# Optimization experiments

Measured on AMD Instinct MI355X. Metric: run time of the kernel, lower is better.

## Reference

```python
import jax, jax.numpy as jnp
import numpy as np

B, N, D, H = 2, 2048, 768, 12
HD = D // H  # head_dim = 64
SCALE = HD ** -0.5


def setup_inputs() -> dict:
    key = jax.random.key(0)
    ks = jax.random.split(key, 8)
    return {
        "x": jax.random.normal(ks[0], (B, N, D), jnp.float32),
        "masks": jax.random.uniform(ks[1], (B, H, N), jnp.float32),
        "lambda_r": jax.random.uniform(ks[2], (B, H), jnp.float32) * 4.0 + 1.0,
        "theta_r": jax.random.uniform(ks[3], (B, H), jnp.float32),
        "mask_weights": jax.random.uniform(ks[4], (B, H), jnp.float32),
        "qkv_w": jax.random.normal(ks[5], (D, 3 * D), jnp.float32) * (D ** -0.5),
        "qkv_b": jnp.zeros((3 * D,), jnp.float32),
        "proj_w": jax.random.normal(ks[6], (D, D), jnp.float32) * (D ** -0.5),
        "proj_b": jnp.zeros((D,), jnp.float32),
    }


def reference(x, masks, lambda_r, theta_r, mask_weights, qkv_w, qkv_b, proj_w, proj_b):
    # qkv projection: [B,N,3D] -> [3,B,H,N,HD]
    qkv = (x @ qkv_w + qkv_b).reshape(B, N, 3, H, HD).transpose(2, 0, 3, 1, 4)
    q, k, v = qkv[0], qkv[1], qkv[2]
    # raw scores [B,H,N,N]
    attn = jnp.einsum('bhqd,bhkd->bhqk', q, k) * SCALE
    # region gate: sigmoid(lambda * (m_i*m_j - theta)) multiplied into scores pre-softmax
    gate = jax.nn.sigmoid(
        lambda_r[:, :, None, None]
        * (masks[:, :, :, None] * masks[:, :, None, :] - theta_r[:, :, None, None])
    )
    attn = jax.nn.softmax(attn * gate, axis=-1)  # dropout is identity in eval
    out = jnp.einsum('bhqk,bhkd->bqhd', attn, v).reshape(B, N, D)
    # per-head output scaling via mask_weights
    out = out * jnp.repeat(mask_weights, HD, axis=-1)[:, None, :]
    return out @ proj_w + proj_b
```

## Files before the change

### kernel.cpp

```cpp
#include <hip/hip_runtime.h>

typedef unsigned short u16;
typedef unsigned int u32;
typedef __attribute__((ext_vector_type(8))) short short8;
typedef __attribute__((ext_vector_type(4))) float f32x4;

#define NB 2
#define NSEQ 2048
#define DIM 768
#define NH 12
#define HDIM 64

#define LOG2E 1.44269504088896f
#define CFOLD 0.18033688f

#if defined(__has_builtin)
#if __has_builtin(__builtin_amdgcn_exp2f)
#define EXPB(x) __builtin_amdgcn_exp2f(x)
#else
#define EXPB(x) exp2f(x)
#endif
#if __has_builtin(__builtin_amdgcn_rcpf)
#define RCP(x) __builtin_amdgcn_rcpf(x)
#else
#define RCP(x) (1.0f / (x))
#endif
#else
#define EXPB(x) exp2f(x)
#define RCP(x) (1.0f / (x))
#endif

__device__ __forceinline__ u16 f2bf(float x) {
    union { float f; unsigned u; } v; v.f = x;
    unsigned r = v.u + 0x7fffu + ((v.u >> 16) & 1u);
    return (u16)(r >> 16);
}

__device__ __forceinline__ u32 pack_bf16(float a, float b) {
    union { float f; u32 u; } A, B; A.f = a; B.f = b;
    u32 ra = A.u + 0x7fffu + ((A.u >> 16) & 1u);
    u32 rb = B.u + 0x7fffu + ((B.u >> 16) & 1u);
    return __builtin_amdgcn_perm(rb, ra, 0x07060302u);
}

__device__ __forceinline__ u32 pack_rtn(float a, float b) {
    union { float f; u32 u; } A, B; A.f = a; B.f = b;
    return __builtin_amdgcn_perm(B.u + 0x8000u, A.u + 0x8000u, 0x07060302u);
}

__device__ __forceinline__ f32x4 mfma16(short8 a, short8 b, f32x4 c) {
    return __builtin_amdgcn_mfma_f32_16x16x32_bf16(a, b, c, 0, 0, 0);
}

__device__ __forceinline__ void glds16(const u16* g, u16* l) {
    __builtin_amdgcn_global_load_lds((const __attribute__((address_space(1))) u32*)g,
                                     (__attribute__((address_space(3))) u32*)l, 16, 0, 0);
}

__global__ __launch_bounds__(256) void prep(const float* __restrict__ x, u16* __restrict__ xb,
                                            const float* __restrict__ qkv_w, u16* __restrict__ wq,
                                            const float* __restrict__ proj_w, u16* __restrict__ wp) {
    const int t = threadIdx.x;
    int bid = blockIdx.x;
    if (bid < 3072) {
        int i = (bid * 256 + t) * 4;
        float4 v = *(const float4*)(x + i);
        *(uint2*)(xb + i) = make_uint2(pack_bf16(v.x, v.y), pack_bf16(v.z, v.w));
        return;
    }
    const float* in; u16* outp; int rows, cols, bx, by;
    if (bid < 3072 + 1728) {
        bid -= 3072; in = qkv_w; outp = wq; rows = 768; cols = 2304;
        bx = bid % 72; by = bid / 72;
    } else {
        bid -= 4800; in = proj_w; outp = wp; rows = 768; cols = 768;
        bx = bid % 24; by = bid / 24;
    }
    __shared__ float tile[32][33];
    int c0 = bx * 32, r0 = by * 32;
    int tx = t & 31, ty = t >> 5;
    #pragma unroll
    for (int i = 0; i < 32; i += 8)
        tile[ty + i][tx] = in[(size_t)(r0 + ty + i) * cols + c0 + tx];
    __syncthreads();
    #pragma unroll
    for (int i = 0; i < 32; i += 8)
        outp[(size_t)(c0 + ty + i) * rows + r0 + tx] = f2bf(tile[tx][ty + i]);
}

__global__ __launch_bounds__(256) void gemm_qkv(const u16* __restrict__ A,
                                                const u16* __restrict__ BT,
                                                const float* __restrict__ bias,
                                                u16* __restrict__ qo,
                                                u16* __restrict__ ko,
                                                u16* __restrict__ vo) {
    __shared__ __align__(16) u16 pool[17408];
    const int bm = blockIdx.y * 128, bn = blockIdx.x * 128;
    const int t = threadIdx.x;
    const int lane = t & 63, wave = t >> 6;
    const int l15 = lane & 15, quad = lane >> 4;
    const int wm = (wave >> 1) * 64, wn = (wave & 1) * 64;

    const int srow = t >> 2;
    const int sc = (t & 3) ^ ((srow >> 1) & 3);
    const u16* ga = A + (size_t)(bm + srow) * DIM + sc * 8;
    const u16* gb = BT + (size_t)(bn + srow) * DIM + sc * 8;
    const int ldst = wave * 512;
    const int swz = (quad ^ ((l15 >> 1) & 3)) * 8;
    u16* As0 = pool;
    u16* Bs0 = pool + 8192;

    f32x4 acc[4][4] = {};
    glds16(ga, As0 + ldst); glds16(ga + (size_t)64 * DIM, As0 + 2048 + ldst);
    glds16(gb, Bs0 + ldst); glds16(gb + (size_t)64 * DIM, Bs0 + 2048 + ldst);
    ga += 32; gb += 32;

    const int NKT = DIM / 32;
    for (int kt = 0; kt < NKT; kt++) {
        const int bo = (kt & 1) * 4096;
        __syncthreads();
        if (kt + 1 < NKT) {
            const int bn2 = (bo ^ 4096);
            glds16(ga, As0 + bn2 + ldst); glds16(ga + (size_t)64 * DIM, As0 + bn2 + 2048 + ldst);
            glds16(gb, Bs0 + bn2 + ldst); glds16(gb + (size_t)64 * DIM, Bs0 + bn2 + 2048 + ldst);
            ga += 32; gb += 32;
        }
        short8 af[4], bf[4];
        #pragma unroll
        for (int i = 0; i < 4; i++) af[i] = *(const short8*)&As0[bo + (wm + i * 16 + l15) * 32 + swz];
        #pragma unroll
        for (int j = 0; j < 4; j++) bf[j] = *(const short8*)&Bs0[bo + (wn + j * 16 + l15) * 32 + swz];
        #pragma unroll
        for (int i = 0; i < 4; i++)
            #pragma unroll
            for (int j = 0; j < 4; j++)
                acc[i][j] = mfma16(af[i], bf[j], acc[i][j]);
    }

    __syncthreads();
    u16* Cs = pool;
    #pragma unroll
    for (int i = 0; i < 4; i++) {
        int row0 = wm + i * 16 + quad * 4;
        #pragma unroll
        for (int j = 0; j < 4; j++) {
            int lcol = wn + j * 16 + l15;
            float bb = bias[bn + lcol];
            #pragma unroll
            for (int r = 0; r < 4; r++)
                Cs[(row0 + r) * 136 + lcol] = f2bf(acc[i][j][r] + bb);
        }
    }
    __syncthreads();

    const int w = bn / DIM;
    const int h0 = (bn - w * DIM) >> 6;
    const int b = bm >> 11, nnb = bm & 2047;
    if (w < 2) {
        u16* dst = w ? ko : qo;
        #pragma unroll
        for (int p = 0; p < 8; p++) {
            int row = p * 16 + (t >> 4);
            int chunk = t & 15;
            short8 v = *(const short8*)&Cs[row * 136 + chunk * 8];
            *(short8*)&dst[(((size_t)(b * NH + h0 + (chunk >> 3))) * NSEQ + nnb + row) * HDIM +
                           (chunk & 7) * 8] = v;
        }
    } else {
        #pragma unroll
        for (int p = 0; p < 8; p++) {
            int hdf = p * 16 + (t >> 4);
            int nn0 = (t & 15) * 8;
            short8 v;
            #pragma unroll
            for (int k = 0; k < 8; k++) v[k] = (short)Cs[(nn0 + k) * 136 + hdf];
            *(short8*)&vo[(((size_t)(b * NH + h0 + (hdf >> 6))) * HDIM + (hdf & 63)) * NSEQ +
                          nnb + nn0] = v;
        }
    }
}

__global__ __launch_bounds__(256) void attn_kernel(const u16* __restrict__ Q,
                                                   const u16* __restrict__ Kg,
                                                   const u16* __restrict__ Vt,
                                                   const float* __restrict__ masks,
                                                   const float* __restrict__ lambda_r,
                                                   const float* __restrict__ theta_r,
                                                   const float* __restrict__ mask_w,
                                                   u16* __restrict__ AO) {
    const int bh = blockIdx.y;
    const int b = bh / NH, h = bh % NH;
    const int qb = blockIdx.x * 64;
    const int t = threadIdx.x, wave = t >> 6, lane = t & 63;
    const int l15 = lane & 15, quad = lane >> 4;

    __shared__ __align__(16) u16 Ks[2][4096];
    __shared__ __align__(16) u16 Vs[2][4096];
    __shared__ __align__(16) u16 Ps[4][1152];
    __shared__ __align__(16) float mks[2][64];

    const float lam = lambda_r[bh], th = theta_r[bh], mw = mask_w[bh];
    const float Bfac = lam * th * LOG2E;

    const size_t base = (size_t)bh * (NSEQ * HDIM);
    const int qrow = qb + wave * 16;

    const u16* Qr = Q + base + (size_t)(qrow + l15) * HDIM;
    short8 bq0 = *(const short8*)(Qr + quad * 8);
    short8 bq1 = *(const short8*)(Qr + 32 + quad * 8);
    const float Afac = -lam * LOG2E * masks[bh * NSEQ + qrow + l15];

    const int srow = t >> 3;
    const int gc = (t & 7) ^ (srow & 7);
    const u16* kgp = Kg + base + (size_t)srow * HDIM + gc * 8;
    const u16* vgp = Vt + base + (size_t)srow * NSEQ + gc * 8;
    const int ldst = wave * 512;

    const int ph = (quad ^ (l15 & 7)) * 8;
    const int kb0 = l15 * 64 + ph, kb1 = l15 * 64 + (ph ^ 32);
    u16* PsW = Ps[wave];
    const int pw = l15 * 72 + quad * 4;
    const int prd = l15 * 72 + quad * 8;
    const float* mrow = masks + bh * NSEQ;

    float lsum = 0.f;
    f32x4 O[4] = {};

    glds16(kgp, &Ks[0][ldst]);
    glds16(kgp + 32 * HDIM, &Ks[0][2048 + ldst]);
    glds16(vgp, &Vs[0][ldst]);
    glds16(vgp + (size_t)32 * NSEQ, &Vs[0][2048 + ldst]);
    if (t < 16) *(float4*)&mks[0][t * 4] = *(const float4*)&mrow[t * 4];

    const int NT = NSEQ / 64;
    for (int kt = 0; kt < NT; kt++) {
        const int buf = kt & 1;
        __syncthreads();
        if (kt + 1 < NT) {
            const u16* kn = kgp + (kt + 1) * 64 * HDIM;
            const u16* vn = vgp + (kt + 1) * 64;
            glds16(kn, &Ks[buf ^ 1][ldst]);
            glds16(kn + 32 * HDIM, &Ks[buf ^ 1][2048 + ldst]);
            glds16(vn, &Vs[buf ^ 1][ldst]);
            glds16(vn + (size_t)32 * NSEQ, &Vs[buf ^ 1][2048 + ldst]);
            if (t < 16) *(float4*)&mks[buf ^ 1][t * 4] = *(const float4*)&mrow[(kt + 1) * 64 + t * 4];
        }
        const u16* KsB = Ks[buf];
        const u16* VsB = Vs[buf];
        const float* mkb = mks[buf];

        float gp[4][4];
        #pragma unroll
        for (int c = 0; c < 4; c++) {
            float4 mkv = *(const float4*)&mkb[c * 16 + quad * 4];
            #pragma unroll
            for (int r = 0; r < 4; r++) {
                float mk = (r == 0) ? mkv.x : (r == 1) ? mkv.y : (r == 2) ? mkv.z : mkv.w;
                float e = EXPB(fmaf(mk, Afac, Bfac));
                gp[c][r] = CFOLD * RCP(1.0f + e);
            }
        }

        #pragma unroll
        for (int c = 0; c < 4; c++) {
            short8 ak0 = *(const short8*)&KsB[kb0 + c * 1024];
            short8 ak1 = *(const short8*)&KsB[kb1 + c * 1024];
            f32x4 S = {0.f, 0.f, 0.f, 0.f};
            S = mfma16(ak0, bq0, S);
            S = mfma16(ak1, bq1, S);
            float p[4];
            #pragma unroll
            for (int r = 0; r < 4; r++) p[r] = EXPB(S[r] * gp[c][r]);
            lsum += (p[0] + p[1]) + (p[2] + p[3]);
            *(uint2*)&PsW[pw + c * 16] = make_uint2(pack_rtn(p[0], p[1]), pack_rtn(p[2], p[3]));
        }

        #pragma unroll
        for (int kc = 0; kc < 2; kc++) {
            const int vb = kc ? kb1 : kb0;
            short8 bp = *(const short8*)&PsW[prd + kc * 32];
            #pragma unroll
            for (int dt = 0; dt < 4; dt++) {
                short8 av = *(const short8*)&VsB[vb + dt * 1024];
                O[dt] = mfma16(av, bp, O[dt]);
            }
        }
    }

    lsum += __shfl_xor(lsum, 16);
    lsum += __shfl_xor(lsum, 32);
    float sc = mw / lsum;
    u16* aor = AO + ((size_t)(b * NSEQ) + qrow + l15) * DIM + h * HDIM + quad * 4;
    #pragma unroll
    for (int dt = 0; dt < 4; dt++) {
        *(uint2*)(aor + dt * 16) = make_uint2(pack_rtn(O[dt][0] * sc, O[dt][1] * sc),
                                              pack_rtn(O[dt][2] * sc, O[dt][3] * sc));
    }
}

__global__ __launch_bounds__(256) void gemm_proj(const u16* __restrict__ A,
                                                 const u16* __restrict__ BT,
                                                 const float* __restrict__ bias,
                                                 float* __restrict__ outp) {
    __shared__ __align__(16) u16 As[2][4096];
    __shared__ __align__(16) u16 Bs[2][2048];
    const int bm = blockIdx.y * 128, bn = blockIdx.x * 64;
    const int t = threadIdx.x;
    const int lane = t & 63, wave = t >> 6;
    const int l15 = lane & 15, quad = lane >> 4;
    const int wm = wave * 32;

    const int srow = t >> 2;
    const int sc = (t & 3) ^ ((srow >> 1) & 3);
    const u16* ga = A + (size_t)(bm + srow) * DIM + sc * 8;
    const u16* gb = BT + (size_t)(bn + srow) * DIM + sc * 8;
    const int ldst = wave * 512;
    const int swz = (quad ^ ((l15 >> 1) & 3)) * 8;

    f32x4 acc[2][4] = {};
    glds16(ga, &As[0][ldst]); glds16(ga + (size_t)64 * DIM, &As[0][2048 + ldst]);
    glds16(gb, &Bs[0][ldst]);
    ga += 32; gb += 32;

    const int NKT = DIM / 32;
    for (int kt = 0; kt < NKT; kt++) {
        const int buf = kt & 1;
        __syncthreads();
        if (kt + 1 < NKT) {
            glds16(ga, &As[buf ^ 1][ldst]); glds16(ga + (size_t)64 * DIM, &As[buf ^ 1][2048 + ldst]);
            glds16(gb, &Bs[buf ^ 1][ldst]);
            ga += 32; gb += 32;
        }
        short8 af[2], bf[4];
        #pragma unroll
        for (int i = 0; i < 2; i++) af[i] = *(const short8*)&As[buf][(wm + i * 16 + l15) * 32 + swz];
        #pragma unroll
        for (int j = 0; j < 4; j++) bf[j] = *(const short8*)&Bs[buf][(j * 16 + l15) * 32 + swz];
        #pragma unroll
        for (int i = 0; i < 2; i++)
            #pragma unroll
            for (int j = 0; j < 4; j++)
                acc[i][j] = mfma16(af[i], bf[j], acc[i][j]);
    }

    #pragma unroll
    for (int i = 0; i < 2; i++) {
        int mr = bm + wm + i * 16 + quad * 4;
        #pragma unroll
        for (int j = 0; j < 4; j++) {
            int ncol = bn + j * 16 + l15;
            float bb = bias[ncol];
            #pragma unroll
            for (int r = 0; r < 4; r++)
                outp[(size_t)(mr + r) * DIM + ncol] = acc[i][j][r] + bb;
        }
    }
}

extern "C" void kernel_launch(void* const* d_in, const int* in_sizes, int n_in,
                              void* d_out, int out_size, void* d_ws, size_t ws_size,
                              hipStream_t stream) {
    const float* x            = (const float*)d_in[0];
    const float* masks        = (const float*)d_in[1];
    const float* lambda_r     = (const float*)d_in[2];
    const float* theta_r      = (const float*)d_in[3];
    const float* mask_weights = (const float*)d_in[4];
    const float* qkv_w        = (const float*)d_in[5];
    const float* qkv_b        = (const float*)d_in[6];
    const float* proj_w       = (const float*)d_in[7];
    const float* proj_b       = (const float*)d_in[8];
    float* outp = (float*)d_out;

    const size_t SZH = (size_t)NB * NH * NSEQ * HDIM;
    u16* xb    = (u16*)d_ws;
    u16* wqkvT = xb + (size_t)4096 * 768;
    u16* wprT  = wqkvT + (size_t)2304 * 768;
    u16* qg    = wprT + (size_t)768 * 768;
    u16* kg    = qg + SZH;
    u16* vt    = kg + SZH;
    u16* ao    = xb;

    prep<<<dim3(3072 + 1728 + 576), 256, 0, stream>>>(x, xb, qkv_w, wqkvT, proj_w, wprT);
    gemm_qkv<<<dim3(2304 / 128, 4096 / 128), 256, 0, stream>>>(xb, wqkvT, qkv_b, qg, kg, vt);
    attn_kernel<<<dim3(NSEQ / 64, NB * NH), 256, 0, stream>>>(qg, kg, vt, masks, lambda_r,
                                                              theta_r, mask_weights, ao);
    gemm_proj<<<dim3(768 / 64, 4096 / 128), 256, 0, stream>>>(ao, wprT, proj_b, outp);
}
```

Measured before the change: 192.4 us.

## Split attention key tiles across wave pairs with LDS reduction of partial outputs

The attention kernel goes to 512 threads. Each pair of waves shares one 16-row query group, and each wave of the pair handles half of every 64-key tile. The partial O accumulators and row sums are combined through shared memory at the end, with one wave of each pair doing the normalised store. This doubles the waves per block and halves each wave's per-tile work to expose more parallelism and latency hiding, at the cost of an extra LDS reduction, more syncs and higher register/LDS pressure per block.

Measured after the change: 186.6 us. 1.03x faster.

```diff
diff --git a/kernel.cpp b/kernel.cpp
--- a/kernel.cpp
+++ b/kernel.cpp
@@ -180,7 +180,7 @@
     }
 }
 
-__global__ __launch_bounds__(256) void attn_kernel(const u16* __restrict__ Q,
+__global__ __launch_bounds__(512) void attn_kernel(const u16* __restrict__ Q,
                                                    const u16* __restrict__ Kg,
                                                    const u16* __restrict__ Vt,
                                                    const float* __restrict__ masks,
@@ -193,17 +193,18 @@
     const int qb = blockIdx.x * 64;
     const int t = threadIdx.x, wave = t >> 6, lane = t & 63;
     const int l15 = lane & 15, quad = lane >> 4;
-
-    __shared__ __align__(16) u16 Ks[2][4096];
-    __shared__ __align__(16) u16 Vs[2][4096];
-    __shared__ __align__(16) u16 Ps[4][1152];
+    const int g = wave >> 1, kh = wave & 1;
+
+    __shared__ __align__(16) u16 pool[16384];
+    __shared__ __align__(16) u16 Ps[8][640];
     __shared__ __align__(16) float mks[2][64];
+    __shared__ float Ls[8][16];
 
     const float lam = lambda_r[bh], th = theta_r[bh], mw = mask_w[bh];
     const float Bfac = lam * th * LOG2E;
 
     const size_t base = (size_t)bh * (NSEQ * HDIM);
-    const int qrow = qb + wave * 16;
+    const int qrow = qb + g * 16;
 
     const u16* Qr = Q + base + (size_t)(qrow + l15) * HDIM;
     short8 bq0 = *(const short8*)(Qr + quad * 8);
@@ -214,45 +215,40 @@
     const int gc = (t & 7) ^ (srow & 7);
     const u16* kgp = Kg + base + (size_t)srow * HDIM + gc * 8;
     const u16* vgp = Vt + base + (size_t)srow * NSEQ + gc * 8;
-    const int ldst = wave * 512;
+    const int wbase = wave * 512;
 
     const int ph = (quad ^ (l15 & 7)) * 8;
-    const int kb0 = l15 * 64 + ph, kb1 = l15 * 64 + (ph ^ 32);
+    const int vph = kh ? (ph ^ 32) : ph;
     u16* PsW = Ps[wave];
-    const int pw = l15 * 72 + quad * 4;
-    const int prd = l15 * 72 + quad * 8;
+    const int pw = l15 * 40 + quad * 4;
+    const int prd = l15 * 40 + quad * 8;
     const float* mrow = masks + bh * NSEQ;
 
     float lsum = 0.f;
     f32x4 O[4] = {};
 
-    glds16(kgp, &Ks[0][ldst]);
-    glds16(kgp + 32 * HDIM, &Ks[0][2048 + ldst]);
-    glds16(vgp, &Vs[0][ldst]);
-    glds16(vgp + (size_t)32 * NSEQ, &Vs[0][2048 + ldst]);
+    glds16(kgp, pool + wbase);
+    glds16(vgp, pool + 8192 + wbase);
     if (t < 16) *(float4*)&mks[0][t * 4] = *(const float4*)&mrow[t * 4];
 
     const int NT = NSEQ / 64;
     for (int kt = 0; kt < NT; kt++) {
-        const int buf = kt & 1;
+        const int bufofs = (kt & 1) * 4096;
         __syncthreads();
         if (kt + 1 < NT) {
-            const u16* kn = kgp + (kt + 1) * 64 * HDIM;
-            const u16* vn = vgp + (kt + 1) * 64;
-            glds16(kn, &Ks[buf ^ 1][ldst]);
-            glds16(kn + 32 * HDIM, &Ks[buf ^ 1][2048 + ldst]);
-            glds16(vn, &Vs[buf ^ 1][ldst]);
-            glds16(vn + (size_t)32 * NSEQ, &Vs[buf ^ 1][2048 + ldst]);
-            if (t < 16) *(float4*)&mks[buf ^ 1][t * 4] = *(const float4*)&mrow[(kt + 1) * 64 + t * 4];
-        }
-        const u16* KsB = Ks[buf];
-        const u16* VsB = Vs[buf];
-        const float* mkb = mks[buf];
-
-        float gp[4][4];
-        #pragma unroll
-        for (int c = 0; c < 4; c++) {
-            float4 mkv = *(const float4*)&mkb[c * 16 + quad * 4];
+            glds16(kgp + (kt + 1) * 64 * HDIM, pool + (bufofs ^ 4096) + wbase);
+            glds16(vgp + (kt + 1) * 64, pool + 8192 + (bufofs ^ 4096) + wbase);
+            if (t < 16) *(float4*)&mks[(kt + 1) & 1][t * 4] =
+                *(const float4*)&mrow[(kt + 1) * 64 + t * 4];
+        }
+        const u16* KsB = pool + bufofs;
+        const u16* VsB = pool + 8192 + bufofs;
+        const float* mkb = mks[kt & 1];
+
+        float gp[2][4];
+        #pragma unroll
+        for (int c = 0; c < 2; c++) {
+            float4 mkv = *(const float4*)&mkb[kh * 32 + c * 16 + quad * 4];
             #pragma unroll
             for (int r = 0; r < 4; r++) {
                 float mk = (r == 0) ? mkv.x : (r == 1) ? mkv.y : (r == 2) ? mkv.z : mkv.w;
@@ -262,9 +258,10 @@
         }
 
         #pragma unroll
-        for (int c = 0; c < 4; c++) {
-            short8 ak0 = *(const short8*)&KsB[kb0 + c * 1024];
-            short8 ak1 = *(const short8*)&KsB[kb1 + c * 1024];
+        for (int c = 0; c < 2; c++) {
+            const int krow = kh * 32 + c * 16 + l15;
+            short8 ak0 = *(const short8*)&KsB[krow * 64 + ph];
+            short8 ak1 = *(const short8*)&KsB[krow * 64 + (ph ^ 32)];
             f32x4 S = {0.f, 0.f, 0.f, 0.f};
             S = mfma16(ak0, bq0, S);
             S = mfma16(ak1, bq1, S);
@@ -275,26 +272,35 @@
             *(uint2*)&PsW[pw + c * 16] = make_uint2(pack_rtn(p[0], p[1]), pack_rtn(p[2], p[3]));
         }
 
-        #pragma unroll
-        for (int kc = 0; kc < 2; kc++) {
-            const int vb = kc ? kb1 : kb0;
-            short8 bp = *(const short8*)&PsW[prd + kc * 32];
-            #pragma unroll
-            for (int dt = 0; dt < 4; dt++) {
-                short8 av = *(const short8*)&VsB[vb + dt * 1024];
-                O[dt] = mfma16(av, bp, O[dt]);
-            }
-        }
-    }
-
-    lsum += __shfl_xor(lsum, 16);
-    lsum += __shfl_xor(lsum, 32);
-    float sc = mw / lsum;
-    u16* aor = AO + ((size_t)(b * NSEQ) + qrow + l15) * DIM + h * HDIM + quad * 4;
-    #pragma unroll
-    for (int dt = 0; dt < 4; dt++) {
-        *(uint2*)(aor + dt * 16) = make_uint2(pack_rtn(O[dt][0] * sc, O[dt][1] * sc),
-                                              pack_rtn(O[dt][2] * sc, O[dt][3] * sc));
+        short8 bp = *(const short8*)&PsW[prd];
+        #pragma unroll
+        for (int dt = 0; dt < 4; dt++) {
+            short8 av = *(const short8*)&VsB[(dt * 16 + l15) * 64 + vph];
+            O[dt] = mfma16(av, bp, O[dt]);
+        }
+    }
+
+    __syncthreads();
+    float* Op = (float*)pool;
+    const int slot = (wave * 64 + lane) * 16;
+    #pragma unroll
+    for (int dt = 0; dt < 4; dt++) *(f32x4*)&Op[slot + dt * 4] = O[dt];
+    float ls = lsum;
+    ls += __shfl_xor(ls, 16);
+    ls += __shfl_xor(ls, 32);
+    if (quad == 0) Ls[wave][l15] = ls;
+    __syncthreads();
+    if (kh == 0) {
+        const int pslot = ((wave ^ 1) * 64 + lane) * 16;
+        float sc = mw / (ls + Ls[wave ^ 1][l15]);
+        u16* aor = AO + ((size_t)(b * NSEQ) + qrow + l15) * DIM + h * HDIM + quad * 4;
+        #pragma unroll
+        for (int dt = 0; dt < 4; dt++) {
+            f32x4 oc = *(const f32x4*)&Op[pslot + dt * 4];
+            float o0 = (O[dt][0] + oc[0]) * sc, o1 = (O[dt][1] + oc[1]) * sc;
+            float o2 = (O[dt][2] + oc[2]) * sc, o3 = (O[dt][3] + oc[3]) * sc;
+            *(uint2*)(aor + dt * 16) = make_uint2(pack_rtn(o0, o1), pack_rtn(o2, o3));
+        }
     }
 }
 
@@ -382,7 +388,7 @@
 
     prep<<<dim3(3072 + 1728 + 576), 256, 0, stream>>>(x, xb, qkv_w, wqkvT, proj_w, wprT);
     gemm_qkv<<<dim3(2304 / 128, 4096 / 128), 256, 0, stream>>>(xb, wqkvT, qkv_b, qg, kg, vt);
-    attn_kernel<<<dim3(NSEQ / 64, NB * NH), 256, 0, stream>>>(qg, kg, vt, masks, lambda_r,
+    attn_kernel<<<dim3(NSEQ / 64, NB * NH), 512, 0, stream>>>(qg, kg, vt, masks, lambda_r,
                                                               theta_r, mask_weights, ao);
     gemm_proj<<<dim3(768 / 64, 4096 / 128), 256, 0, stream>>>(ao, wprT, proj_b, outp);
 }
```
